# Kernel tuning notes

Hardware: AMD Instinct MI355X
Metric: run time of the kernel (lower is better)

The kernel has to match this reference:

```python
import jax, jax.numpy as jnp
import numpy as np

PATCH_SIZE = 9
EPS = 1e-05


def to_patches(x, p):
    # x: [b, c, H, W] -> [b, c*(H-p+1)*(W-p+1), p, p]
    # matches torch unfold(2,p,1).unfold(3,p,1) + rearrange 'b c p1 p2 h w -> b (c p1 p2) h w'
    b, c, H, W = x.shape
    Hp, Wp = H - p + 1, W - p + 1
    # fixed small loop over p*p offsets (p=9); XLA fuses these slices
    pat = jnp.stack([x[:, :, i:i + Hp, j:j + Wp] for i in range(p) for j in range(p)], axis=2)
    pat = pat.reshape(b, c, p, p, Hp, Wp)
    pat = jnp.transpose(pat, (0, 1, 4, 5, 2, 3))  # b c Hp Wp p p
    return pat.reshape(b, c * Hp * Wp, p, p)


def _norm(x, eps):
    # per-channel normalization over last two dims (population variance, correction=0)
    mu = jnp.mean(x, axis=(-1, -2), keepdims=True)
    var = jnp.mean((x - mu) ** 2, axis=(-1, -2), keepdims=True) + eps
    return (x - mu) / jnp.sqrt(var)


def setup_inputs() -> dict:
    key = jax.random.key(0)
    k1, k2, k3 = jax.random.split(key, 3)
    b, c, H, W, p = 8, 1, 128, 128, PATCH_SIZE
    Hp, Wp = H - p + 1, W - p + 1
    x1 = jax.random.normal(k1, (b, c, H, W), dtype=jnp.float32)
    x2 = jax.random.normal(k2, (b, c, H, W), dtype=jnp.float32)
    mask2 = jax.random.uniform(k3, (b, c * Hp * Wp, p, p), dtype=jnp.float32)
    return {"x1": x1, "x2": x2, "mask2": mask2}


def reference(x1, x2, mask2):
    p = PATCH_SIZE
    x1p = to_patches(x1, p)
    x2p = to_patches(x2, p)
    _, c, h, w = x1p.shape
    x2p = x2p * mask2
    x1n = _norm(x1p, EPS)
    x2n = _norm(x2p, EPS)
    score = jnp.einsum('bchw,bchw->b', x1n, x2n)
    return score / (c * h * w)
```

## Files before the change

### kernel.cpp

```cpp
#include <hip/hip_runtime.h>


#define BATCH 8
#define HH    128
#define WW    128
#define PP    9
#define HP    120
#define WP    120
#define NPATCH (HP * WP)
#define PSQ   (PP * PP)
#define EPSF  1e-5f
#define CHUNKP 60
#define CHUNKF (CHUNKP * PSQ)
#define NBLK  (BATCH * HP / 2)

__device__ __forceinline__ void gload16(const void* g, void* lds) {
    __builtin_amdgcn_global_load_lds(
        (const __attribute__((address_space(1))) void*)g,
        (__attribute__((address_space(3))) void*)lds, 16, 0, 0);
}

__global__ __launch_bounds__(128) void ncc_kernel(const float* __restrict__ x1,
                                                  const float* __restrict__ x2,
                                                  const float* __restrict__ mask,
                                                  float* __restrict__ part)
{
    const int blk  = blockIdx.x;
    const int b    = blk / 60;
    const int i0   = (blk - b * 60) * 2;
    const int tid  = threadIdx.x;
    const int lane = tid & 63;

    __shared__ __align__(16) float m_lds[2][CHUNKF];
    __shared__ __align__(16) float x_lds[2][10 * WW];
    __shared__ float wsum[2];

    {
        const float4* s1 = (const float4*)(x1 + ((size_t)(b * HH + i0)) * WW);
        const float4* s2 = (const float4*)(x2 + ((size_t)(b * HH + i0)) * WW);
        char* d1 = (char*)&x_lds[0][0];
        char* d2 = (char*)&x_lds[1][0];
        #pragma unroll
        for (int k = 0; k < 3; ++k) {
            int t = k * 128 + tid;
            if (t < 320) {
                gload16(s1 + t, d1 + (size_t)(t - lane) * 16);
                gload16(s2 + t, d2 + (size_t)(t - lane) * 16);
            }
        }
    }

    auto stage_mask = [&](int k) {
        const int row = i0 + (k >> 1);
        const int jh  = k & 1;
        const float4* msrc = (const float4*)(
            mask + ((size_t)b * NPATCH + (size_t)row * WP + CHUNKP * jh) * PSQ);
        char* mdst = (char*)&m_lds[k & 1][0];
        #pragma unroll
        for (int q = 0; q < 10; ++q) {
            int t = q * 128 + tid;
            if (t < CHUNKF / 4)
                gload16(msrc + t, mdst + (size_t)(t - lane) * 16);
        }
    };

    stage_mask(0);

    float val = 0.0f;
    #pragma unroll
    for (int k = 0; k < 4; ++k) {
        __syncthreads();
        if (k < 3) stage_mask(k + 1);

        const int pl = tid >> 1;
        const int h  = tid & 1;
        if (pl < CHUNKP) {
            const int r2 = k >> 1;
            const int j  = CHUNKP * (k & 1) + pl;
            const int rr0 = h ? 5 : 0;
            const int rr1 = h ? 9 : 5;
            float sa = 0.f, saa = 0.f, sb = 0.f, sbb = 0.f, sab = 0.f;
            const float* mp = &m_lds[k & 1][pl * PSQ + rr0 * PP];
            for (int r = rr0; r < rr1; ++r) {
                const float* x1r = &x_lds[0][(r2 + r) * WW + j];
                const float* x2r = &x_lds[1][(r2 + r) * WW + j];
                #pragma unroll
                for (int cc = 0; cc < PP; ++cc) {
                    float a  = x1r[cc];
                    float bv = x2r[cc] * mp[cc];
                    sa += a;  saa = fmaf(a, a, saa);
                    sb += bv; sbb = fmaf(bv, bv, sbb);
                    sab = fmaf(a, bv, sab);
                }
                mp += PP;
            }
            sa  += __shfl_xor(sa, 1);
            saa += __shfl_xor(saa, 1);
            sb  += __shfl_xor(sb, 1);
            sbb += __shfl_xor(sbb, 1);
            sab += __shfl_xor(sab, 1);
            if (h == 0) {
                const float invN = 1.0f / 81.0f;
                float mua  = sa * invN;
                float mub  = sb * invN;
                float vara = saa * invN - mua * mua + EPSF;
                float varb = sbb * invN - mub * mub + EPSF;
                float cov  = sab - 81.0f * mua * mub;
                val += cov / sqrtf(vara * varb);
            }
        }
    }

    #pragma unroll
    for (int off = 32; off > 0; off >>= 1)
        val += __shfl_down(val, off);
    if ((tid & 63) == 0) wsum[tid >> 6] = val;
    __syncthreads();
    if (tid == 0)
        part[blk] = wsum[0] + wsum[1];
}

__global__ __launch_bounds__(64) void finalize_kernel(const float* __restrict__ part,
                                                      float* __restrict__ out)
{
    const int b = blockIdx.x;
    const int t = threadIdx.x;
    float v = (t < 60) ? part[b * 60 + t] : 0.0f;
    #pragma unroll
    for (int off = 32; off > 0; off >>= 1)
        v += __shfl_down(v, off);
    if (t == 0)
        out[b] = v * (1.0f / ((float)NPATCH * (float)PSQ));
}

extern "C" void kernel_launch(void* const* d_in, const int* in_sizes, int n_in,
                              void* d_out, int out_size, void* d_ws, size_t ws_size,
                              hipStream_t stream) {
    const float* x1   = (const float*)d_in[0];
    const float* x2   = (const float*)d_in[1];
    const float* mask = (const float*)d_in[2];
    float* out  = (float*)d_out;
    float* part = (float*)d_ws;

    ncc_kernel<<<NBLK, 128, 0, stream>>>(x1, x2, mask, part);
    finalize_kernel<<<BATCH, 64, 0, stream>>>(part, out);
}
```

Measured before the change: 19.16 us.

## Widen blocks to 256 threads, stage full mask rows, pack x1/x2/x1*x2 in LDS

Each block now uses 256 threads, so one pass covers all 120 patch columns of an output row, and the whole row's mask is staged into LDS at once instead of in four half-row chunks. The x1 and x2 image rows are loaded through registers and packed into float4 entries (a, b, a*b) so each inner-loop step does one vector LDS read and reuses the precomputed product. Mask double buffering is gone: the second row's mask is loaded only after a barrier, which serializes that load with compute and may expose its latency. The packed LDS layout is also twice the size of the old x buffers and may lower occupancy.

```diff
diff --git a/kernel.cpp b/kernel.cpp
--- a/kernel.cpp
+++ b/kernel.cpp
@@ -10,8 +10,6 @@
 #define NPATCH (HP * WP)
 #define PSQ   (PP * PP)
 #define EPSF  1e-5f
-#define CHUNKP 60
-#define CHUNKF (CHUNKP * PSQ)
 #define NBLK  (BATCH * HP / 2)
 
 __device__ __forceinline__ void gload16(const void* g, void* lds) {
@@ -20,7 +18,7 @@
         (__attribute__((address_space(3))) void*)lds, 16, 0, 0);
 }
 
-__global__ __launch_bounds__(128) void ncc_kernel(const float* __restrict__ x1,
+__global__ __launch_bounds__(256) void ncc_kernel(const float* __restrict__ x1,
                                                   const float* __restrict__ x2,
                                                   const float* __restrict__ mask,
                                                   float* __restrict__ part)
@@ -31,68 +29,65 @@
     const int tid  = threadIdx.x;
     const int lane = tid & 63;
 
-    __shared__ __align__(16) float m_lds[2][CHUNKF];
-    __shared__ __align__(16) float x_lds[2][10 * WW];
-    __shared__ float wsum[2];
+    __shared__ __align__(16) float  m_lds[WP * PSQ];
+    __shared__ __align__(16) float4 pk[10 * WW];
+    __shared__ float wsum[4];
+
+    auto stage_mask = [&](int ri) {
+        const float4* msrc = (const float4*)(
+            mask + ((size_t)b * NPATCH + (size_t)ri * WP) * PSQ);
+        char* mdst = (char*)m_lds;
+        #pragma unroll
+        for (int k = 0; k < 10; ++k) {
+            int t = k * 256 + tid;
+            if (t < (WP * PSQ) / 4)
+                gload16(msrc + t, mdst + (size_t)(t - lane) * 16);
+        }
+    };
+    stage_mask(i0);
 
     {
         const float4* s1 = (const float4*)(x1 + ((size_t)(b * HH + i0)) * WW);
         const float4* s2 = (const float4*)(x2 + ((size_t)(b * HH + i0)) * WW);
-        char* d1 = (char*)&x_lds[0][0];
-        char* d2 = (char*)&x_lds[1][0];
         #pragma unroll
-        for (int k = 0; k < 3; ++k) {
-            int t = k * 128 + tid;
+        for (int k = 0; k < 2; ++k) {
+            int t = k * 256 + tid;
             if (t < 320) {
-                gload16(s1 + t, d1 + (size_t)(t - lane) * 16);
-                gload16(s2 + t, d2 + (size_t)(t - lane) * 16);
+                float4 a = s1[t];
+                float4 c = s2[t];
+                pk[t * 4 + 0] = make_float4(a.x, c.x, a.x * c.x, 0.f);
+                pk[t * 4 + 1] = make_float4(a.y, c.y, a.y * c.y, 0.f);
+                pk[t * 4 + 2] = make_float4(a.z, c.z, a.z * c.z, 0.f);
+                pk[t * 4 + 3] = make_float4(a.w, c.w, a.w * c.w, 0.f);
             }
         }
     }
 
-    auto stage_mask = [&](int k) {
-        const int row = i0 + (k >> 1);
-        const int jh  = k & 1;
-        const float4* msrc = (const float4*)(
-            mask + ((size_t)b * NPATCH + (size_t)row * WP + CHUNKP * jh) * PSQ);
-        char* mdst = (char*)&m_lds[k & 1][0];
-        #pragma unroll
-        for (int q = 0; q < 10; ++q) {
-            int t = q * 128 + tid;
-            if (t < CHUNKF / 4)
-                gload16(msrc + t, mdst + (size_t)(t - lane) * 16);
-        }
-    };
-
-    stage_mask(0);
-
     float val = 0.0f;
     #pragma unroll
-    for (int k = 0; k < 4; ++k) {
+    for (int rr = 0; rr < 2; ++rr) {
         __syncthreads();
-        if (k < 3) stage_mask(k + 1);
 
-        const int pl = tid >> 1;
-        const int h  = tid & 1;
-        if (pl < CHUNKP) {
-            const int r2 = k >> 1;
-            const int j  = CHUNKP * (k & 1) + pl;
-            const int rr0 = h ? 5 : 0;
-            const int rr1 = h ? 9 : 5;
+        const int j = tid >> 1;
+        const int h = tid & 1;
+        if (j < WP) {
+            const int r0 = h ? 5 : 0;
+            const int r1 = h ? 9 : 5;
             float sa = 0.f, saa = 0.f, sb = 0.f, sbb = 0.f, sab = 0.f;
-            const float* mp = &m_lds[k & 1][pl * PSQ + rr0 * PP];
-            for (int r = rr0; r < rr1; ++r) {
-                const float* x1r = &x_lds[0][(r2 + r) * WW + j];
-                const float* x2r = &x_lds[1][(r2 + r) * WW + j];
+            const float*  mp  = m_lds + j * PSQ + r0 * PP;
+            const float4* pkb = &pk[(rr + r0) * WW + j];
+            for (int r = r0; r < r1; ++r) {
                 #pragma unroll
                 for (int cc = 0; cc < PP; ++cc) {
-                    float a  = x1r[cc];
-                    float bv = x2r[cc] * mp[cc];
-                    sa += a;  saa = fmaf(a, a, saa);
-                    sb += bv; sbb = fmaf(bv, bv, sbb);
-                    sab = fmaf(a, bv, sab);
+                    float4 v = pkb[cc];
+                    float  m = mp[cc];
+                    float  bv = v.y * m;
+                    sa += v.x;  saa = fmaf(v.x, v.x, saa);
+                    sb += bv;   sbb = fmaf(bv, bv, sbb);
+                    sab = fmaf(v.z, m, sab);
                 }
-                mp += PP;
+                mp  += PP;
+                pkb += WW;
             }
             sa  += __shfl_xor(sa, 1);
             saa += __shfl_xor(saa, 1);
@@ -109,6 +104,11 @@
                 val += cov / sqrtf(vara * varb);
             }
         }
+
+        if (rr == 0) {
+            __syncthreads();
+            stage_mask(i0 + 1);
+        }
     }
 
     #pragma unroll
@@ -117,7 +117,7 @@
     if ((tid & 63) == 0) wsum[tid >> 6] = val;
     __syncthreads();
     if (tid == 0)
-        part[blk] = wsum[0] + wsum[1];
+        part[blk] = wsum[0] + wsum[1] + wsum[2] + wsum[3];
 }
 
 __global__ __launch_bounds__(64) void finalize_kernel(const float* __restrict__ part,
@@ -142,6 +142,6 @@
     float* out  = (float*)d_out;
     float* part = (float*)d_ws;
 
-    ncc_kernel<<<NBLK, 128, 0, stream>>>(x1, x2, mask, part);
+    ncc_kernel<<<NBLK, 256, 0, stream>>>(x1, x2, mask, part);
     finalize_kernel<<<BATCH, 64, 0, stream>>>(part, out);
 }
```

After: 18.17 us. -5.2%, faster.
